# Kernel optimization log

Hardware: AMD Instinct MI355X
Metric: run time of the kernel (lower is better)

## Reference

```python
import jax, jax.numpy as jnp
import numpy as np
import math

EPS = 1e-7
N, M, K, D_IN, D_OUT = 8192, 32, 8, 64, 64
KP_EXTENT = 0.66

# ---- Lorentz manifold (curvature k = 1) helpers ----

def l_inner(x, y):
    # Lorentzian inner product, keepdim on last axis
    return -x[..., :1] * y[..., :1] + jnp.sum(x[..., 1:] * y[..., 1:], axis=-1, keepdims=True)

def l_dist(x, y):
    alpha = jnp.clip(-l_inner(x, y), 1.0 + EPS, None)
    return jnp.arccosh(alpha)[..., 0]

def expmap0(u):
    # u: tangent at origin, time component ignored-by-construction (zero)
    sp = u[..., 1:]
    un = jnp.sqrt(jnp.clip(jnp.sum(sp * sp, axis=-1, keepdims=True), 1e-14, None))
    return jnp.concatenate([jnp.cosh(un), jnp.sinh(un) * sp / un], axis=-1)

def expmap(x, u):
    un = jnp.sqrt(jnp.clip(l_inner(u, u), 1e-14, None))
    return jnp.cosh(un) * x + jnp.sinh(un) * u / un

def logmap(x, y):
    alpha = jnp.clip(-l_inner(x, y), 1.0 + EPS, None)
    d = jnp.arccosh(alpha)
    nom = y - alpha * x
    den = jnp.sqrt(jnp.clip(alpha * alpha - 1.0, 1e-14, None))
    return d * nom / den

def ptransp(x, y, v):
    # parallel transport of v from x to y
    return v + l_inner(y, v) / (1.0 - l_inner(x, y)) * (x + y)

def norm_midpoint(ave):
    den = jnp.sqrt(jnp.clip(jnp.abs(l_inner(ave, ave)), 1e-8, None))
    return ave / den


def setup_inputs() -> dict:
    key = jax.random.key(0)
    k1, k2, k3, k4, k5, k6 = jax.random.split(key, 6)
    # points on the hyperboloid: time = sqrt(1 + ||space||^2)
    sp = jax.random.normal(k1, (N, D_IN - 1), dtype=jnp.float32) * 0.5
    t = jnp.sqrt(1.0 + jnp.sum(sp * sp, axis=-1, keepdims=True))
    x = jnp.concatenate([t, sp], axis=-1)
    nei = jax.random.randint(k2, (N, M), 0, N, dtype=jnp.int32)
    nei_mask = jax.random.randint(k3, (N, M), 0, 2, dtype=jnp.int32)
    # kernel points: tangent vectors at origin (time comp 0), first point = center
    kp_sp = jax.random.normal(k4, (K, D_IN - 1), dtype=jnp.float32)
    kp_sp = kp_sp / jnp.linalg.norm(kp_sp, axis=-1, keepdims=True)
    radii = jax.random.uniform(k5, (K, 1), dtype=jnp.float32) * KP_EXTENT
    kp_sp = kp_sp * radii
    kp_sp = kp_sp.at[0].set(0.0)
    kernel_points = jnp.concatenate([jnp.zeros((K, 1), jnp.float32), kp_sp], axis=-1)
    # K LorentzLinear params
    stdv = 1.0 / math.sqrt(D_OUT)
    W = jax.random.uniform(k6, (K, D_OUT, D_IN), dtype=jnp.float32, minval=-stdv, maxval=stdv)
    W = W.at[:, :, 0].set(0.0)  # reset_parameters zeros first input column
    b = jnp.zeros((K, D_OUT), dtype=jnp.float32)
    scale = jnp.full((K,), math.log(10.0), dtype=jnp.float32)
    return {"x": x, "nei": nei, "nei_mask": nei_mask, "W": W, "b": b,
            "scale": scale, "kernel_points": kernel_points}


def reference(x, nei, nei_mask, W, b, scale, kernel_points):
    n, d = x.shape
    x_nei = x[nei]                      # [n, m, d] gather
    xr = x[:, None, :]                  # [n, 1, d]
    og_row = jnp.zeros((d,), x.dtype).at[0].set(1.0)
    # transport_x: map each neighborhood to the origin's tangent frame
    v = logmap(xr, x_nei)
    x0_nei = expmap0(ptransp(xr, og_row[None, None, :], v))   # [n, m, d]
    # kernel positions at the origin (transp=True => base point is origin)
    tmp = expmap(og_row[None, :], ptransp(og_row[None, :], og_row[None, :], kernel_points[1:]))
    x_kernel = jnp.concatenate([tmp, og_row[None, :]], axis=0)  # [K, d]
    # geodesic distances neighbor <-> kernel point: [n, K, m]
    dis = l_dist(x0_nei[:, None, :, :], x_kernel[None, :, None, :])
    dis = dis * nei_mask[:, None, :].astype(x.dtype)
    # K LorentzLinear transforms (vectorized over K): [n, K, m, d_out]
    h = jnp.einsum('nmd,kod->nkmo', x0_nei, W) + b[None, :, None, :]
    time = jax.nn.sigmoid(h[..., :1]) * jnp.exp(scale)[None, :, None, None] + 1.0001
    nar = h[..., 1:]
    s = (time * time - 1.0) / jnp.clip(jnp.sum(nar * nar, axis=-1, keepdims=True), 1e-8, None)
    xt = jnp.concatenate([time, nar * jnp.sqrt(s)], axis=-1)
    # weighted Lorentz midpoint over kernel points, per neighbor: [n, m, d_out]
    per_nei = norm_midpoint(jnp.einsum('nkm,nkmo->nmo', dis, xt))
    # unweighted Lorentz midpoint over neighbors: [n, d_out]
    return norm_midpoint(per_nei.mean(axis=1))
```

## Files before the change

### kernel.cpp

```cpp
#include <hip/hip_runtime.h>
#include <hip/hip_bf16.h>

#define N_NODES 8192
#define M_NEI   32
#define K_PTS   8
#define D       64
#define EPS_    1e-7f

typedef float f4v __attribute__((ext_vector_type(4)));
typedef short s8v __attribute__((ext_vector_type(8)));

__device__ __forceinline__ ushort f2bf(float f) {
  __hip_bfloat16 h = __float2bfloat16(f);
  return *reinterpret_cast<ushort*>(&h);
}
__device__ __forceinline__ float bf2f(ushort u) {
  __hip_bfloat16 h;
  *reinterpret_cast<ushort*>(&h) = u;
  return __bfloat162float(h);
}
__device__ __forceinline__ float frcp(float x)  { return __builtin_amdgcn_rcpf(x); }
__device__ __forceinline__ float frsq(float x)  { return __builtin_amdgcn_rsqf(x); }
__device__ __forceinline__ float fsqrt(float x) { return __builtin_amdgcn_sqrtf(x); }
__device__ __forceinline__ float facosh(float a) {
  float den = fsqrt(fmaxf(a * a - 1.f, 1e-14f));
  return __logf(a + den);
}

template<int CTRL>
__device__ __forceinline__ float dppadd(float v) {
  int t = __builtin_amdgcn_update_dpp(0, __float_as_int(v), CTRL, 0xf, 0xf, true);
  return v + __int_as_float(t);
}
template<int CTRL>
__device__ __forceinline__ float dppmov(float v) {
  return __int_as_float(__builtin_amdgcn_update_dpp(0, __float_as_int(v), CTRL, 0xf, 0xf, true));
}
__device__ __forceinline__ float swz_xor4(float v) {
  return __int_as_float(__builtin_amdgcn_ds_swizzle(__float_as_int(v), 0x101F));
}
__device__ __forceinline__ float sum8(float v) {
  v = dppadd<0xB1>(v);
  v = dppadd<0x4E>(v);
  v = dppadd<0x141>(v);
  return v;
}
__device__ __forceinline__ float sum16(float v) {
  v = dppadd<0x121>(v);
  v = dppadd<0x122>(v);
  v = dppadd<0x124>(v);
  v = dppadd<0x128>(v);
  return v;
}

__global__ void prep_xk(const float* __restrict__ kp, const float* __restrict__ scale,
                        float* __restrict__ xk) {
  int d = threadIdx.x;
  for (int kk = 0; kk < K_PTS - 1; ++kk) {
    float v = kp[(kk + 1) * D + d];
    float p = (d == 0) ? 0.f : v * v;
    #pragma unroll
    for (int s = 1; s < 64; s <<= 1) p += __shfl_xor(p, s);
    float un = sqrtf(fmaxf(p, 1e-14f));
    float sh = sinhf(un) / un;
    xk[kk * D + d] = (d == 0) ? coshf(un) : sh * v;
  }
  xk[(K_PTS - 1) * D + d] = (d == 0) ? 1.f : 0.f;
  if (d < K_PTS) xk[K_PTS * D + d] = expf(scale[d]);
}

__global__ void prep_wb(const float* __restrict__ W, ushort* __restrict__ WF) {
  int idx = blockIdx.x * 256 + threadIdx.x;
  int k    = idx >> 9;
  int ct   = (idx >> 7) & 3;
  int ks   = (idx >> 6) & 1;
  int lane = idx & 63;
  int o  = ct * 16 + (lane & 15);
  int db = (lane >> 4) * 8 + ks * 32;
  const float* wrow = W + (k * 64 + o) * 64 + db;
  s8v hi, lo;
  #pragma unroll
  for (int j = 0; j < 8; ++j) {
    float w = wrow[j];
    ushort h = f2bf(w);
    hi[j] = (short)h;
    lo[j] = (short)f2bf(w - bf2f(h));
  }
  int f = (k * 4 + ct) * 2 + ks;
  *(s8v*)(WF + (size_t)(f * 2 + 0) * 512 + lane * 8) = hi;
  *(s8v*)(WF + (size_t)(f * 2 + 1) * 512 + lane * 8) = lo;
}

__launch_bounds__(256, 4)
__global__ void kpa_main(const float* __restrict__ x, const int* __restrict__ nei,
                         const int* __restrict__ mask, const ushort* __restrict__ WF,
                         const float* __restrict__ b, const float* __restrict__ scale,
                         const float* __restrict__ xk, float* __restrict__ out) {
  __shared__ __align__(16) float  xr_s[D];
  __shared__ __align__(16) float  xk_s[K_PTS * D];
  __shared__ __align__(16) ushort Ah_lds[M_NEI * D];
  __shared__ __align__(16) ushort Al_lds[M_NEI * D];
  __shared__ float dis_s[K_PTS * 33];
  __shared__ __align__(8)  float  hss[K_PTS * M_NEI * 2];
  __shared__ __align__(8)  float  dm2[K_PTS * M_NEI * 2];
  __shared__ __align__(16) float  red_w[2][M_NEI * 68];
  __shared__ __align__(16) float  redp[4 * D];

  const int n  = blockIdx.x;
  const int t  = threadIdx.x;
  const int w4 = t >> 6;
  const int l  = t & 63;
  const int cl = l & 15;
  const int gr = l >> 4;
  const int wm = w4 & 1;
  const int wk = w4 >> 1;

  if (t < D) xr_s[t] = x[n * D + t];
  xk_s[t] = xk[t]; xk_s[t + 256] = xk[t + 256];
  __syncthreads();

  {
    const int m  = t >> 3;
    const int l8 = t & 7;
    const int d0 = l8 * 8;
    const int ni = nei[n * M_NEI + m];
    float y[8], xr[8];
    float y0 = x[ni * D];
    {
      float4 ya = *(const float4*)(x + ni * D + d0);
      float4 yb = *(const float4*)(x + ni * D + d0 + 4);
      y[0]=ya.x; y[1]=ya.y; y[2]=ya.z; y[3]=ya.w;
      y[4]=yb.x; y[5]=yb.y; y[6]=yb.z; y[7]=yb.w;
      float4 ra = *(const float4*)(xr_s + d0);
      float4 rb = *(const float4*)(xr_s + d0 + 4);
      xr[0]=ra.x; xr[1]=ra.y; xr[2]=ra.z; xr[3]=ra.w;
      xr[4]=rb.x; xr[5]=rb.y; xr[6]=rb.z; xr[7]=rb.w;
    }
    const float xr0 = xr_s[0];
    float p = 0.f;
    #pragma unroll
    for (int j = 0; j < 8; ++j) p += xr[j] * y[j];
    if (l8 == 0) p -= 2.f * xr[0] * y[0];
    p = sum8(p);
    float alpha = fmaxf(-p, 1.f + EPS_);
    float den = fsqrt(fmaxf(alpha * alpha - 1.f, 1e-14f));
    float dd  = __logf(alpha + den);
    float f   = dd * frcp(den);
    float v[8];
    #pragma unroll
    for (int j = 0; j < 8; ++j) v[j] = f * (y[j] - alpha * xr[j]);
    float v0 = f * (y0 - alpha * xr0);
    float c  = -v0 * frcp(1.f + xr0);
    float wv[8];
    float q = 0.f;
    #pragma unroll
    for (int j = 0; j < 8; ++j) { wv[j] = v[j] + c * xr[j]; q += wv[j] * wv[j]; }
    if (l8 == 0) q -= wv[0] * wv[0];
    q = sum8(q);
    float un = fsqrt(fmaxf(q, 1e-14f));
    float e  = __expf(un);
    float ei = frcp(e);
    float sh = (0.5f * (e - ei)) * frcp(un);
    float x0v[8];
    #pragma unroll
    for (int j = 0; j < 8; ++j) x0v[j] = sh * wv[j];
    if (l8 == 0) x0v[0] = 0.5f * (e + ei);
    {
      s8v hi, lo;
      #pragma unroll
      for (int j = 0; j < 8; ++j) {
        uint u = __float_as_uint(x0v[j]);
        hi[j] = (short)(ushort)(u >> 16);
        float lof = x0v[j] - __uint_as_float(u & 0xffff0000u);
        uint ul = __float_as_uint(lof);
        lo[j] = (short)(ushort)((ul + 0x7fffu + ((ul >> 16) & 1u)) >> 16);
      }
      int byte = m * 128 + d0 * 2;
      int swz  = byte ^ ((m & 7) << 4);
      *(s8v*)((char*)Ah_lds + swz) = hi;
      *(s8v*)((char*)Al_lds + swz) = lo;
    }
    float msk = (float)mask[n * M_NEI + m];
    if (l8 == 0) x0v[0] = -x0v[0];
    float pk[8];
    #pragma unroll
    for (int kk = 0; kk < K_PTS; ++kk) {
      const float* xkp = xk_s + kk * D + d0;
      float pp = 0.f;
      #pragma unroll
      for (int j = 0; j < 8; ++j) pp += x0v[j] * xkp[j];
      pk[kk] = pp;
    }
    const bool hi4 = (l8 & 4);
    float s1[4];
    #pragma unroll
    for (int j = 0; j < 4; ++j) {
      float give = hi4 ? pk[j] : pk[j + 4];
      float keep = hi4 ? pk[j + 4] : pk[j];
      s1[j] = keep + swz_xor4(give);
    }
    const bool hi2 = (l8 & 2);
    float s2[2];
    #pragma unroll
    for (int j = 0; j < 2; ++j) {
      float give = hi2 ? s1[j] : s1[j + 2];
      float keep = hi2 ? s1[j + 2] : s1[j];
      s2[j] = keep + dppmov<0x4E>(give);
    }
    const bool hi1 = (l8 & 1);
    float give = hi1 ? s2[0] : s2[1];
    float keep = hi1 ? s2[1] : s2[0];
    float mypp = keep + dppmov<0xB1>(give);
    float al_ = fmaxf(-mypp, 1.f + EPS_);
    dis_s[l8 * 33 + m] = facosh(al_) * msk;
  }
  __syncthreads();

  const int row = wm * 16 + cl;
  s8v ah[2], alo[2];
  #pragma unroll
  for (int ks = 0; ks < 2; ++ks) {
    int byte = row * 128 + (gr * 8 + ks * 32) * 2;
    int swz  = byte ^ ((row & 7) << 4);
    ah[ks]  = *(const s8v*)((const char*)Ah_lds + swz);
    alo[ks] = *(const s8v*)((const char*)Al_lds + swz);
  }

  f4v acc[4][4];
  #pragma unroll
  for (int kq = 0; kq < 4; ++kq) {
    const int k = wk * 4 + kq;
    #pragma unroll
    for (int ct = 0; ct < 4; ++ct) {
      float bv = b[k * 64 + ct * 16 + cl];
      f4v a = (f4v){bv, bv, bv, bv};
      #pragma unroll
      for (int ks = 0; ks < 2; ++ks) {
        int fi = (k * 4 + ct) * 2 + ks;
        s8v bh = *(const s8v*)(WF + (size_t)(fi * 2 + 0) * 512 + l * 8);
        s8v bl = *(const s8v*)(WF + (size_t)(fi * 2 + 1) * 512 + l * 8);
        a = __builtin_amdgcn_mfma_f32_16x16x32_bf16(ah[ks],  bh, a, 0, 0, 0);
        a = __builtin_amdgcn_mfma_f32_16x16x32_bf16(ah[ks],  bl, a, 0, 0, 0);
        a = __builtin_amdgcn_mfma_f32_16x16x32_bf16(alo[ks], bh, a, 0, 0, 0);
      }
      acc[kq][ct] = a;
    }
    #pragma unroll
    for (int r = 0; r < 4; ++r) {
      float ss = acc[kq][0][r]*acc[kq][0][r] + acc[kq][1][r]*acc[kq][1][r]
               + acc[kq][2][r]*acc[kq][2][r] + acc[kq][3][r]*acc[kq][3][r];
      ss = sum16(ss);
      if (cl == 0) {
        const int m = wm * 16 + gr * 4 + r;
        float2* hp = (float2*)&hss[(k * M_NEI + m) * 2];
        *hp = make_float2(acc[kq][0][r], ss);
      }
    }
  }
  __syncthreads();

  {
    const int k = t >> 5;
    const int m = t & 31;
    float2 hp = *(const float2*)&hss[(k * M_NEI + m) * 2];
    float h0 = hp.x, ss = hp.y;
    float nar2 = fmaxf(ss - h0 * h0, 1e-8f);
    float es   = xk[K_PTS * D + k];
    float time = es * frcp(1.f + __expf(-h0)) + 1.0001f;
    float sq   = fsqrt(time * time - 1.f) * frsq(nar2);
    float dm   = dis_s[k * 33 + m];
    *(float2*)&dm2[(k * M_NEI + m) * 2] = make_float2(dm * sq, dm * time);
  }
  __syncthreads();

  float yacc[4][4];
  #pragma unroll
  for (int r = 0; r < 4; ++r)
    #pragma unroll
    for (int ct = 0; ct < 4; ++ct) yacc[r][ct] = 0.f;

  #pragma unroll
  for (int kq = 0; kq < 4; ++kq) {
    const int k = wk * 4 + kq;
    #pragma unroll
    for (int r = 0; r < 4; ++r) {
      const int m = wm * 16 + gr * 4 + r;
      float2 dd = *(const float2*)&dm2[(k * M_NEI + m) * 2];
      yacc[r][0] += (cl == 0) ? dd.y : dd.x * acc[kq][0][r];
      yacc[r][1] += dd.x * acc[kq][1][r];
      yacc[r][2] += dd.x * acc[kq][2][r];
      yacc[r][3] += dd.x * acc[kq][3][r];
    }
  }
  #pragma unroll
  for (int r = 0; r < 4; ++r) {
    const int m = wm * 16 + gr * 4 + r;
    float* rw = &red_w[wk][m * 68];
    rw[cl]      = yacc[r][0];
    rw[16 + cl] = yacc[r][1];
    rw[32 + cl] = yacc[r][2];
    rw[48 + cl] = yacc[r][3];
  }
  __syncthreads();

  {
    const int m  = t >> 3;
    const int l8 = t & 7;
    const int o0 = l8 * 8;
    f4v s0 = *(const f4v*)&red_w[0][m * 68 + o0]     + *(const f4v*)&red_w[1][m * 68 + o0];
    f4v s1 = *(const f4v*)&red_w[0][m * 68 + o0 + 4] + *(const f4v*)&red_w[1][m * 68 + o0 + 4];
    float v[8] = {s0.x, s0.y, s0.z, s0.w, s1.x, s1.y, s1.z, s1.w};
    float ip = 0.f;
    #pragma unroll
    for (int j = 0; j < 8; ++j) ip += v[j] * v[j];
    if (l8 == 0) ip -= 2.f * v[0] * v[0];
    ip = sum8(ip);
    float rin = frsq(fmaxf(fabsf(ip), 1e-8f));
    #pragma unroll
    for (int j = 0; j < 8; ++j) {
      float z = v[j] * rin;
      z = dppadd<0x128>(z);
      z += __shfl_xor(z, 16); z += __shfl_xor(z, 32);
      v[j] = z;
    }
    if (l < 8) {
      #pragma unroll
      for (int j = 0; j < 8; ++j) redp[w4 * D + l8 * 8 + j] = v[j];
    }
  }
  __syncthreads();
  if (t < D) {
    float mv = (redp[t] + redp[D + t] + redp[2 * D + t] + redp[3 * D + t]) * (1.f / 32.f);
    float ip = (t == 0) ? -mv * mv : mv * mv;
    ip = sum8(ip);
    ip = dppadd<0x128>(ip);
    ip += __shfl_xor(ip, 16); ip += __shfl_xor(ip, 32);
    out[n * D + t] = mv * frsq(fmaxf(fabsf(ip), 1e-8f));
  }
}

extern "C" void kernel_launch(void* const* d_in, const int* in_sizes, int n_in,
                              void* d_out, int out_size, void* d_ws, size_t ws_size,
                              hipStream_t stream) {
  const float* x     = (const float*)d_in[0];
  const int*   nei   = (const int*)d_in[1];
  const int*   mask  = (const int*)d_in[2];
  const float* W     = (const float*)d_in[3];
  const float* b     = (const float*)d_in[4];
  const float* scale = (const float*)d_in[5];
  const float* kp    = (const float*)d_in[6];
  float* out = (float*)d_out;

  ushort* WF = (ushort*)d_ws;
  float*  xk = (float*)(WF + 65536);

  prep_wb<<<16, 256, 0, stream>>>(W, WF);
  prep_xk<<<1, 64, 0, stream>>>(kp, scale, xk);
  kpa_main<<<N_NODES, 256, 0, stream>>>(x, nei, mask, WF, b, scale, xk, out);
}
```

Before: 104.5 us.

## Shrink LDS footprint and restructure final midpoint reductions to raise occupancy

Reuses the hss buffer for the distance-scaled coefficients instead of a separate dm2 array. It replaces the full cross-wave LDS reduction with a half-sized exchange: the wk==1 waves write their partials and the wk==0 waves combine them in registers, normalize, and reduce. A final 16-thread stage writes the output. Launch bounds go from 4 to 6 blocks per SIMD, trading a tighter register budget (spill risk) for more resident blocks; sum16 is assumed to exist in the unseen helpers.

```diff
diff --git a/kernel.cpp b/kernel.cpp
--- a/kernel.cpp
+++ b/kernel.cpp
@@ -91,7 +91,7 @@
   *(s8v*)(WF + (size_t)(f * 2 + 1) * 512 + lane * 8) = lo;
 }
 
-__launch_bounds__(256, 4)
+__launch_bounds__(256, 6)
 __global__ void kpa_main(const float* __restrict__ x, const int* __restrict__ nei,
                          const int* __restrict__ mask, const ushort* __restrict__ WF,
                          const float* __restrict__ b, const float* __restrict__ scale,
@@ -102,9 +102,8 @@
   __shared__ __align__(16) ushort Al_lds[M_NEI * D];
   __shared__ float dis_s[K_PTS * 33];
   __shared__ __align__(8)  float  hss[K_PTS * M_NEI * 2];
-  __shared__ __align__(8)  float  dm2[K_PTS * M_NEI * 2];
-  __shared__ __align__(16) float  red_w[2][M_NEI * 68];
-  __shared__ __align__(16) float  redp[4 * D];
+  __shared__ __align__(16) float  red_h[2][16 * 68];
+  __shared__ __align__(16) float  redp2[2][64];
 
   const int n  = blockIdx.x;
   const int t  = threadIdx.x;
@@ -269,7 +268,7 @@
     float time = es * frcp(1.f + __expf(-h0)) + 1.0001f;
     float sq   = fsqrt(time * time - 1.f) * frsq(nar2);
     float dm   = dis_s[k * 33 + m];
-    *(float2*)&dm2[(k * M_NEI + m) * 2] = make_float2(dm * sq, dm * time);
+    *(float2*)&hss[(k * M_NEI + m) * 2] = make_float2(dm * sq, dm * time);
   }
   __syncthreads();
 
@@ -285,57 +284,69 @@
     #pragma unroll
     for (int r = 0; r < 4; ++r) {
       const int m = wm * 16 + gr * 4 + r;
-      float2 dd = *(const float2*)&dm2[(k * M_NEI + m) * 2];
+      float2 dd = *(const float2*)&hss[(k * M_NEI + m) * 2];
       yacc[r][0] += (cl == 0) ? dd.y : dd.x * acc[kq][0][r];
       yacc[r][1] += dd.x * acc[kq][1][r];
       yacc[r][2] += dd.x * acc[kq][2][r];
       yacc[r][3] += dd.x * acc[kq][3][r];
     }
   }
-  #pragma unroll
-  for (int r = 0; r < 4; ++r) {
-    const int m = wm * 16 + gr * 4 + r;
-    float* rw = &red_w[wk][m * 68];
-    rw[cl]      = yacc[r][0];
-    rw[16 + cl] = yacc[r][1];
-    rw[32 + cl] = yacc[r][2];
-    rw[48 + cl] = yacc[r][3];
-  }
-  __syncthreads();
-
-  {
-    const int m  = t >> 3;
-    const int l8 = t & 7;
-    const int o0 = l8 * 8;
-    f4v s0 = *(const f4v*)&red_w[0][m * 68 + o0]     + *(const f4v*)&red_w[1][m * 68 + o0];
-    f4v s1 = *(const f4v*)&red_w[0][m * 68 + o0 + 4] + *(const f4v*)&red_w[1][m * 68 + o0 + 4];
-    float v[8] = {s0.x, s0.y, s0.z, s0.w, s1.x, s1.y, s1.z, s1.w};
-    float ip = 0.f;
-    #pragma unroll
-    for (int j = 0; j < 8; ++j) ip += v[j] * v[j];
-    if (l8 == 0) ip -= 2.f * v[0] * v[0];
-    ip = sum8(ip);
+
+  if (wk == 1) {
+    #pragma unroll
+    for (int r = 0; r < 4; ++r) {
+      const int ml = gr * 4 + r;
+      float* rw = &red_h[wm][ml * 68];
+      rw[cl]      = yacc[r][0];
+      rw[16 + cl] = yacc[r][1];
+      rw[32 + cl] = yacc[r][2];
+      rw[48 + cl] = yacc[r][3];
+    }
+  }
+  __syncthreads();
+
+  if (wk == 0) {
+    float s[4] = {0.f, 0.f, 0.f, 0.f};
+    #pragma unroll
+    for (int r = 0; r < 4; ++r) {
+      const int ml = gr * 4 + r;
+      const float* rw = &red_h[wm][ml * 68];
+      float v0_ = yacc[r][0] + rw[cl];
+      float v1_ = yacc[r][1] + rw[16 + cl];
+      float v2_ = yacc[r][2] + rw[32 + cl];
+      float v3_ = yacc[r][3] + rw[48 + cl];
+      float ip = v0_*v0_ + v1_*v1_ + v2_*v2_ + v3_*v3_;
+      if (cl == 0) ip -= 2.f * v0_ * v0_;
+      ip = sum16(ip);
+      float rin = frsq(fmaxf(fabsf(ip), 1e-8f));
+      s[0] += v0_ * rin; s[1] += v1_ * rin;
+      s[2] += v2_ * rin; s[3] += v3_ * rin;
+    }
+    #pragma unroll
+    for (int j = 0; j < 4; ++j) {
+      float z = s[j];
+      z += __shfl_xor(z, 16); z += __shfl_xor(z, 32);
+      s[j] = z;
+    }
+    if (gr == 0) {
+      #pragma unroll
+      for (int j = 0; j < 4; ++j) redp2[wm][j * 16 + cl] = s[j];
+    }
+  }
+  __syncthreads();
+
+  if (t < 16) {
+    float mv[4]; float ip = 0.f;
+    #pragma unroll
+    for (int j = 0; j < 4; ++j) {
+      mv[j] = (redp2[0][j * 16 + t] + redp2[1][j * 16 + t]) * (1.f / 32.f);
+      ip += mv[j] * mv[j];
+    }
+    if (t == 0) ip -= 2.f * mv[0] * mv[0];
+    ip = sum16(ip);
     float rin = frsq(fmaxf(fabsf(ip), 1e-8f));
     #pragma unroll
-    for (int j = 0; j < 8; ++j) {
-      float z = v[j] * rin;
-      z = dppadd<0x128>(z);
-      z += __shfl_xor(z, 16); z += __shfl_xor(z, 32);
-      v[j] = z;
-    }
-    if (l < 8) {
-      #pragma unroll
-      for (int j = 0; j < 8; ++j) redp[w4 * D + l8 * 8 + j] = v[j];
-    }
-  }
-  __syncthreads();
-  if (t < D) {
-    float mv = (redp[t] + redp[D + t] + redp[2 * D + t] + redp[3 * D + t]) * (1.f / 32.f);
-    float ip = (t == 0) ? -mv * mv : mv * mv;
-    ip = sum8(ip);
-    ip = dppadd<0x128>(ip);
-    ip += __shfl_xor(ip, 16); ip += __shfl_xor(ip, 32);
-    out[n * D + t] = mv * frsq(fmaxf(fabsf(ip), 1e-8f));
+    for (int j = 0; j < 4; ++j) out[n * D + j * 16 + t] = mv[j] * rin;
   }
 }
 
```

Result: slower. 210.7 us (+101.5%).
